# Performance work log

Hardware: AMD Instinct MI355X
Metric: run time of the kernel (lower is better)

Reference implementation:

```python
import jax, jax.numpy as jnp
import numpy as np

EPS = 1e-8  # torch CosineSimilarity default eps

def _normalize(x):
    # torch clamps each norm at eps before dividing
    n = jnp.sqrt(jnp.sum(x * x, axis=-1, keepdims=True))
    return x / jnp.maximum(n, EPS)

def _cross_entropy(logits, labels):
    logp = jax.nn.log_softmax(logits, axis=-1)
    return -jnp.mean(jnp.take_along_axis(logp, labels[:, None], axis=-1))

def setup_inputs() -> dict:
    key = jax.random.key(0)
    ks = jax.random.split(key, 7)
    B, M, D = 8192, 3129, 512
    return {
        'mm_proj': jax.random.normal(ks[0], (B, D), jnp.float32),
        'ans_embedding': jax.random.normal(ks[1], (M, D), jnp.float32),
        'v_max': jax.random.normal(ks[2], (B, D), jnp.float32),
        'mm': jax.random.normal(ks[3], (B, D), jnp.float32),
        'logits_q': jax.random.normal(ks[4], (B, M), jnp.float32),
        'logits_rubi': jax.random.normal(ks[5], (B, M), jnp.float32),
        'class_id': jax.random.randint(ks[6], (B, 1), 0, M, jnp.int64),
    }

def reference(mm_proj, ans_embedding, v_max, mm, logits_q, logits_rubi, class_id,
              question_loss_weight=1.0):
    cid = class_id.squeeze(1)  # [B]
    # NCE over cosine similarities: fuse normalize + GEMM instead of [B,M,D] expand
    g = _normalize(mm_proj)          # [B, D]
    a = _normalize(ans_embedding)    # [M, D]
    d_logit = jnp.einsum('bd,md->bm', g, a)  # [B, M] cosine matrix
    positive_dist = jnp.take_along_axis(d_logit, cid[:, None], axis=1)[:, 0]  # [B]
    num = jnp.exp(positive_dist)
    den = jnp.sum(jnp.exp(d_logit), axis=-1)
    loss_nce = jnp.mean(-jnp.log(num / den))
    # object cosine loss
    obj_dist = jnp.sum(_normalize(v_max) * _normalize(mm), axis=-1)  # [B]
    obj_loss = jnp.mean(1.0 - obj_dist)
    fusion_loss = (_cross_entropy(logits_rubi, cid) + obj_loss + loss_nce) / 3.0
    question_loss = _cross_entropy(logits_q, cid)
    loss = fusion_loss + question_loss_weight * question_loss
    # out['loss'], out['loss_mm_q'], out['loss_q']
    return jnp.stack([loss, fusion_loss, question_loss])
```

## Files before the change

kernel.cpp:

```cpp
#include <hip/hip_runtime.h>
#include <hip/hip_bf16.h>

#define B_N 8192
#define M_N 3129
#define M_PAD 3200
#define D_N 512

#define GLOBAL_AS __attribute__((address_space(1)))
#define LDS_AS __attribute__((address_space(3)))

typedef __bf16 bf16x8 __attribute__((ext_vector_type(8)));
typedef float f32x4 __attribute__((ext_vector_type(4)));

__global__ __launch_bounds__(256) void normalize_kernel(
    const float* __restrict__ x, __bf16* __restrict__ y,
    int nrows_src, int nrows_out) {
  int wid = threadIdx.x >> 6, lane = threadIdx.x & 63;
  int row = blockIdx.x * 4 + wid;
  if (row >= nrows_out) return;
  bf16x8 out;
  if (row >= nrows_src) {
    for (int j = 0; j < 8; ++j) out[j] = (__bf16)0.0f;
    *(bf16x8*)(y + (size_t)row * D_N + lane * 8) = out;
    return;
  }
  const float4* xr = (const float4*)(x + (size_t)row * D_N);
  float4 v0 = xr[lane * 2], v1 = xr[lane * 2 + 1];
  float s = v0.x*v0.x + v0.y*v0.y + v0.z*v0.z + v0.w*v0.w
          + v1.x*v1.x + v1.y*v1.y + v1.z*v1.z + v1.w*v1.w;
  for (int o = 1; o < 64; o <<= 1) s += __shfl_xor(s, o);
  float rn = 1.0f / fmaxf(sqrtf(s), 1e-8f);
  float vals[8] = {v0.x, v0.y, v0.z, v0.w, v1.x, v1.y, v1.z, v1.w};
  for (int j = 0; j < 8; ++j) out[j] = (__bf16)(vals[j] * rn);
  *(bf16x8*)(y + (size_t)row * D_N + lane * 8) = out;
}

__global__ __launch_bounds__(256) void pos_kernel(
    const __bf16* __restrict__ g, const __bf16* __restrict__ a,
    const int* __restrict__ cid, float* __restrict__ pos) {
  int wid = threadIdx.x >> 6, lane = threadIdx.x & 63;
  int b = blockIdx.x * 4 + wid;
  if (b >= B_N) return;
  int label = cid[b];
  bf16x8 gv = *(const bf16x8*)(g + (size_t)b * D_N + lane * 8);
  bf16x8 av = *(const bf16x8*)(a + (size_t)label * D_N + lane * 8);
  float s = 0.0f;
  for (int j = 0; j < 8; ++j) s += (float)gv[j] * (float)av[j];
  for (int o = 1; o < 64; o <<= 1) s += __shfl_xor(s, o);
  if (lane == 0) pos[b] = s;
}

__global__ __launch_bounds__(256) void nce_gemm_kernel(
    const __bf16* __restrict__ g, const __bf16* __restrict__ a,
    float* __restrict__ den) {
  __shared__ __bf16 As[128 * 32];
  __shared__ __bf16 Bs[128 * 32];
  const int t = threadIdx.x;
  const int mtile = blockIdx.x;
  const int btile = blockIdx.y;
  const int brow0 = btile * 128;
  const int mrow0 = mtile * 128;
  const int lane = t & 63;
  const int wid = t >> 6;
  const int wrow = wid >> 1;
  const int wcol = wid & 1;
  const int r = lane & 15;
  const int quad = lane >> 4;

  f32x4 acc[4][4];
  for (int i = 0; i < 4; ++i)
    for (int j = 0; j < 4; ++j)
      acc[i][j] = f32x4{0.f, 0.f, 0.f, 0.f};

  for (int k0 = 0; k0 < D_N; k0 += 32) {
    __syncthreads();
    for (int i = 0; i < 2; ++i) {
      int s = t + i * 256;
      int row = s >> 2;
      int kq = (s & 3) << 3;
      const __bf16* ga = g + (size_t)(brow0 + row) * D_N + (k0 + kq);
      __builtin_amdgcn_global_load_lds((const GLOBAL_AS void*)ga,
                                       (LDS_AS void*)(As + s * 8), 16, 0, 0);
      const __bf16* gb = a + (size_t)(mrow0 + row) * D_N + (k0 + kq);
      __builtin_amdgcn_global_load_lds((const GLOBAL_AS void*)gb,
                                       (LDS_AS void*)(Bs + s * 8), 16, 0, 0);
    }
    __syncthreads();
    bf16x8 af[4], bf[4];
    for (int i = 0; i < 4; ++i)
      af[i] = *(const bf16x8*)(As + (wrow * 64 + i * 16 + r) * 32 + quad * 8);
    for (int j = 0; j < 4; ++j)
      bf[j] = *(const bf16x8*)(Bs + (wcol * 64 + j * 16 + r) * 32 + quad * 8);
    for (int i = 0; i < 4; ++i)
      for (int j = 0; j < 4; ++j)
        acc[i][j] = __builtin_amdgcn_mfma_f32_16x16x32_bf16(af[i], bf[j],
                                                            acc[i][j], 0, 0, 0);
  }

  for (int i = 0; i < 4; ++i) {
    for (int reg = 0; reg < 4; ++reg) {
      float s = 0.0f;
      for (int j = 0; j < 4; ++j) {
        int m = mrow0 + wcol * 64 + j * 16 + r;
        float v = acc[i][j][reg];
        if (m < M_N) s += __expf(v);
      }
      s += __shfl_xor(s, 1);
      s += __shfl_xor(s, 2);
      s += __shfl_xor(s, 4);
      s += __shfl_xor(s, 8);
      if (r == 0) {
        int b = brow0 + wrow * 64 + i * 16 + quad * 4 + reg;
        atomicAdd(den + b, s);
      }
    }
  }
}

__global__ __launch_bounds__(256) void obj_kernel(
    const float* __restrict__ v, const float* __restrict__ m,
    float* __restrict__ obj) {
  int wid = threadIdx.x >> 6, lane = threadIdx.x & 63;
  int b = blockIdx.x * 4 + wid;
  if (b >= B_N) return;
  const float4* vr = (const float4*)(v + (size_t)b * D_N);
  const float4* mr = (const float4*)(m + (size_t)b * D_N);
  float4 a0 = vr[lane * 2], a1 = vr[lane * 2 + 1];
  float4 b0 = mr[lane * 2], b1 = mr[lane * 2 + 1];
  float sv = a0.x*a0.x + a0.y*a0.y + a0.z*a0.z + a0.w*a0.w
           + a1.x*a1.x + a1.y*a1.y + a1.z*a1.z + a1.w*a1.w;
  float sm = b0.x*b0.x + b0.y*b0.y + b0.z*b0.z + b0.w*b0.w
           + b1.x*b1.x + b1.y*b1.y + b1.z*b1.z + b1.w*b1.w;
  float sd = a0.x*b0.x + a0.y*b0.y + a0.z*b0.z + a0.w*b0.w
           + a1.x*b1.x + a1.y*b1.y + a1.z*b1.z + a1.w*b1.w;
  for (int o = 1; o < 64; o <<= 1) {
    sv += __shfl_xor(sv, o);
    sm += __shfl_xor(sm, o);
    sd += __shfl_xor(sd, o);
  }
  if (lane == 0) {
    float dist = sd / (fmaxf(sqrtf(sv), 1e-8f) * fmaxf(sqrtf(sm), 1e-8f));
    obj[b] = 1.0f - dist;
  }
}

__global__ __launch_bounds__(256) void ce_kernel(
    const float* __restrict__ lq, const float* __restrict__ lr,
    const int* __restrict__ cid,
    float* __restrict__ ce_q, float* __restrict__ ce_r) {
  int b = blockIdx.x;
  const float* rq = lq + (size_t)b * M_N;
  const float* rr = lr + (size_t)b * M_N;
  int t = threadIdx.x;
  int mis = (int)(((size_t)b * M_N) & 3);
  int h = (4 - mis) & 3;
  int n4 = (M_N - h) >> 2;
  int tail0 = h + (n4 << 2);
  int ntail = M_N - tail0;
  float sq = 0.0f, sr = 0.0f;
  if (t < h) { sq += __expf(rq[t]); sr += __expf(rr[t]); }
  if (t >= 64 && t < 64 + ntail) {
    int i = tail0 + (t - 64);
    sq += __expf(rq[i]); sr += __expf(rr[i]);
  }
  const float4* q4 = (const float4*)(rq + h);
  const float4* r4 = (const float4*)(rr + h);
  for (int i = t; i < n4; i += 256) {
    float4 a = q4[i];
    float4 c = r4[i];
    sq += __expf(a.x) + __expf(a.y) + __expf(a.z) + __expf(a.w);
    sr += __expf(c.x) + __expf(c.y) + __expf(c.z) + __expf(c.w);
  }
  for (int o = 1; o < 64; o <<= 1) {
    sq += __shfl_xor(sq, o);
    sr += __shfl_xor(sr, o);
  }
  __shared__ float ssq[4], ssr[4];
  int wid = t >> 6;
  if ((t & 63) == 0) { ssq[wid] = sq; ssr[wid] = sr; }
  __syncthreads();
  if (t == 0) {
    float tq = ssq[0] + ssq[1] + ssq[2] + ssq[3];
    float tr = ssr[0] + ssr[1] + ssr[2] + ssr[3];
    int label = cid[b];
    ce_q[b] = logf(tq) - rq[label];
    ce_r[b] = logf(tr) - rr[label];
  }
}

__global__ __launch_bounds__(256) void final_kernel(
    const float* __restrict__ den, const float* __restrict__ pos,
    const float* __restrict__ ce_q, const float* __restrict__ ce_r,
    const float* __restrict__ obj, float* __restrict__ out) {
  int t = threadIdx.x;
  float s_nce = 0.0f, s_ceq = 0.0f, s_cer = 0.0f, s_obj = 0.0f;
  for (int b = t; b < B_N; b += 256) {
    s_nce += logf(den[b]) - pos[b];
    s_ceq += ce_q[b];
    s_cer += ce_r[b];
    s_obj += obj[b];
  }
  for (int o = 1; o < 64; o <<= 1) {
    s_nce += __shfl_xor(s_nce, o);
    s_ceq += __shfl_xor(s_ceq, o);
    s_cer += __shfl_xor(s_cer, o);
    s_obj += __shfl_xor(s_obj, o);
  }
  __shared__ float red[4][4];
  int wid = t >> 6;
  if ((t & 63) == 0) {
    red[wid][0] = s_nce; red[wid][1] = s_ceq;
    red[wid][2] = s_cer; red[wid][3] = s_obj;
  }
  __syncthreads();
  if (t == 0) {
    float nce = (red[0][0] + red[1][0] + red[2][0] + red[3][0]) / (float)B_N;
    float ceq = (red[0][1] + red[1][1] + red[2][1] + red[3][1]) / (float)B_N;
    float cer = (red[0][2] + red[1][2] + red[2][2] + red[3][2]) / (float)B_N;
    float ob  = (red[0][3] + red[1][3] + red[2][3] + red[3][3]) / (float)B_N;
    float fusion = (cer + ob + nce) * (1.0f / 3.0f);
    float loss = fusion + ceq;
    out[0] = loss;
    out[1] = fusion;
    out[2] = ceq;
  }
}

extern "C" void kernel_launch(void* const* d_in, const int* in_sizes, int n_in,
                              void* d_out, int out_size, void* d_ws, size_t ws_size,
                              hipStream_t stream) {
  const float* mm_proj     = (const float*)d_in[0];
  const float* ans_emb     = (const float*)d_in[1];
  const float* v_max       = (const float*)d_in[2];
  const float* mm          = (const float*)d_in[3];
  const float* logits_q    = (const float*)d_in[4];
  const float* logits_rubi = (const float*)d_in[5];
  const int*   cid         = (const int*)d_in[6];
  float* out = (float*)d_out;

  char* ws = (char*)d_ws;
  __bf16* g = (__bf16*)ws;
  __bf16* a = (__bf16*)(ws + 8388608);
  float* den  = (float*)(ws + 8388608 + 3276800);
  float* pos  = den + B_N;
  float* ce_q = pos + B_N;
  float* ce_r = ce_q + B_N;
  float* obj  = ce_r + B_N;

  hipMemsetAsync(den, 0, (size_t)B_N * sizeof(float), stream);

  normalize_kernel<<<B_N / 4, 256, 0, stream>>>(mm_proj, g, B_N, B_N);
  normalize_kernel<<<M_PAD / 4, 256, 0, stream>>>(ans_emb, a, M_N, M_PAD);
  pos_kernel<<<B_N / 4, 256, 0, stream>>>(g, a, cid, pos);
  nce_gemm_kernel<<<dim3(M_PAD / 128, B_N / 128), 256, 0, stream>>>(g, a, den);
  obj_kernel<<<B_N / 4, 256, 0, stream>>>(v_max, mm, obj);
  ce_kernel<<<B_N, 256, 0, stream>>>(logits_q, logits_rubi, cid, ce_q, ce_r);
  final_kernel<<<1, 256, 0, stream>>>(den, pos, ce_q, ce_r, obj, out);
}
```

Before: 340.2 us.

## Fuse prep kernels, stage CE rows via LDS async loads, parallelize final reduction

Merges the two normalize launches and the object-cosine kernel into one prep kernel to cut launch count. Rewrites the cross-entropy kernel to copy each logits row into LDS with global_load_lds from an aligned start and mask the edges, replacing the scalar head/tail handling. Splits the single-block final reduction into a multi-block atomic reduce plus a tiny combine kernel. This adds two launches at the end, atomic float ordering nondeterminism, and heavy LDS use per CE block that may lower occupancy.

Result: faster. 325.1 us (-4.4%).

```diff
diff --git a/kernel.cpp b/kernel.cpp
--- a/kernel.cpp
+++ b/kernel.cpp
@@ -12,12 +12,13 @@
 typedef __bf16 bf16x8 __attribute__((ext_vector_type(8)));
 typedef float f32x4 __attribute__((ext_vector_type(4)));
 
-__global__ __launch_bounds__(256) void normalize_kernel(
+#define PREP_G_BLOCKS   (B_N / 4)
+#define PREP_A_BLOCKS   (M_PAD / 4)
+#define PREP_OBJ_BLOCKS (B_N / 4)
+
+__device__ __forceinline__ void normalize_row(
     const float* __restrict__ x, __bf16* __restrict__ y,
-    int nrows_src, int nrows_out) {
-  int wid = threadIdx.x >> 6, lane = threadIdx.x & 63;
-  int row = blockIdx.x * 4 + wid;
-  if (row >= nrows_out) return;
+    int row, int nrows_src, int lane) {
   bf16x8 out;
   if (row >= nrows_src) {
     for (int j = 0; j < 8; ++j) out[j] = (__bf16)0.0f;
@@ -33,6 +34,41 @@
   float vals[8] = {v0.x, v0.y, v0.z, v0.w, v1.x, v1.y, v1.z, v1.w};
   for (int j = 0; j < 8; ++j) out[j] = (__bf16)(vals[j] * rn);
   *(bf16x8*)(y + (size_t)row * D_N + lane * 8) = out;
+}
+
+__global__ __launch_bounds__(256) void prep_kernel(
+    const float* __restrict__ mm_proj, const float* __restrict__ ans_emb,
+    const float* __restrict__ v_max, const float* __restrict__ mm,
+    __bf16* __restrict__ g, __bf16* __restrict__ a,
+    float* __restrict__ obj) {
+  int blk = blockIdx.x;
+  int wid = threadIdx.x >> 6, lane = threadIdx.x & 63;
+  if (blk < PREP_G_BLOCKS) {
+    normalize_row(mm_proj, g, blk * 4 + wid, B_N, lane);
+  } else if (blk < PREP_G_BLOCKS + PREP_A_BLOCKS) {
+    normalize_row(ans_emb, a, (blk - PREP_G_BLOCKS) * 4 + wid, M_N, lane);
+  } else {
+    int b = (blk - PREP_G_BLOCKS - PREP_A_BLOCKS) * 4 + wid;
+    const float4* vr = (const float4*)(v_max + (size_t)b * D_N);
+    const float4* mr = (const float4*)(mm + (size_t)b * D_N);
+    float4 a0 = vr[lane * 2], a1 = vr[lane * 2 + 1];
+    float4 b0 = mr[lane * 2], b1 = mr[lane * 2 + 1];
+    float sv = a0.x*a0.x + a0.y*a0.y + a0.z*a0.z + a0.w*a0.w
+             + a1.x*a1.x + a1.y*a1.y + a1.z*a1.z + a1.w*a1.w;
+    float sm = b0.x*b0.x + b0.y*b0.y + b0.z*b0.z + b0.w*b0.w
+             + b1.x*b1.x + b1.y*b1.y + b1.z*b1.z + b1.w*b1.w;
+    float sd = a0.x*b0.x + a0.y*b0.y + a0.z*b0.z + a0.w*b0.w
+             + a1.x*b1.x + a1.y*b1.y + a1.z*b1.z + a1.w*b1.w;
+    for (int o = 1; o < 64; o <<= 1) {
+      sv += __shfl_xor(sv, o);
+      sm += __shfl_xor(sm, o);
+      sd += __shfl_xor(sd, o);
+    }
+    if (lane == 0) {
+      float dist = sd / (fmaxf(sqrtf(sv), 1e-8f) * fmaxf(sqrtf(sm), 1e-8f));
+      obj[b] = 1.0f - dist;
+    }
+  }
 }
 
 __global__ __launch_bounds__(256) void pos_kernel(
@@ -56,10 +92,8 @@
   __shared__ __bf16 As[128 * 32];
   __shared__ __bf16 Bs[128 * 32];
   const int t = threadIdx.x;
-  const int mtile = blockIdx.x;
-  const int btile = blockIdx.y;
-  const int brow0 = btile * 128;
-  const int mrow0 = mtile * 128;
+  const int brow0 = blockIdx.y * 128;
+  const int mrow0 = blockIdx.x * 128;
   const int lane = t & 63;
   const int wid = t >> 6;
   const int wrow = wid >> 1;
@@ -102,8 +136,7 @@
       float s = 0.0f;
       for (int j = 0; j < 4; ++j) {
         int m = mrow0 + wcol * 64 + j * 16 + r;
-        float v = acc[i][j][reg];
-        if (m < M_N) s += __expf(v);
+        if (m < M_N) s += __expf(acc[i][j][reg]);
       }
       s += __shfl_xor(s, 1);
       s += __shfl_xor(s, 2);
@@ -117,59 +150,55 @@
   }
 }
 
-__global__ __launch_bounds__(256) void obj_kernel(
-    const float* __restrict__ v, const float* __restrict__ m,
-    float* __restrict__ obj) {
-  int wid = threadIdx.x >> 6, lane = threadIdx.x & 63;
-  int b = blockIdx.x * 4 + wid;
-  if (b >= B_N) return;
-  const float4* vr = (const float4*)(v + (size_t)b * D_N);
-  const float4* mr = (const float4*)(m + (size_t)b * D_N);
-  float4 a0 = vr[lane * 2], a1 = vr[lane * 2 + 1];
-  float4 b0 = mr[lane * 2], b1 = mr[lane * 2 + 1];
-  float sv = a0.x*a0.x + a0.y*a0.y + a0.z*a0.z + a0.w*a0.w
-           + a1.x*a1.x + a1.y*a1.y + a1.z*a1.z + a1.w*a1.w;
-  float sm = b0.x*b0.x + b0.y*b0.y + b0.z*b0.z + b0.w*b0.w
-           + b1.x*b1.x + b1.y*b1.y + b1.z*b1.z + b1.w*b1.w;
-  float sd = a0.x*b0.x + a0.y*b0.y + a0.z*b0.z + a0.w*b0.w
-           + a1.x*b1.x + a1.y*b1.y + a1.z*b1.z + a1.w*b1.w;
-  for (int o = 1; o < 64; o <<= 1) {
-    sv += __shfl_xor(sv, o);
-    sm += __shfl_xor(sm, o);
-    sd += __shfl_xor(sd, o);
-  }
-  if (lane == 0) {
-    float dist = sd / (fmaxf(sqrtf(sv), 1e-8f) * fmaxf(sqrtf(sm), 1e-8f));
-    obj[b] = 1.0f - dist;
-  }
-}
+#define CE_CHUNKS 784
 
 __global__ __launch_bounds__(256) void ce_kernel(
     const float* __restrict__ lq, const float* __restrict__ lr,
     const int* __restrict__ cid,
     float* __restrict__ ce_q, float* __restrict__ ce_r) {
-  int b = blockIdx.x;
-  const float* rq = lq + (size_t)b * M_N;
-  const float* rr = lr + (size_t)b * M_N;
-  int t = threadIdx.x;
-  int mis = (int)(((size_t)b * M_N) & 3);
-  int h = (4 - mis) & 3;
-  int n4 = (M_N - h) >> 2;
-  int tail0 = h + (n4 << 2);
-  int ntail = M_N - tail0;
+  __shared__ float Lq[CE_CHUNKS * 4];
+  __shared__ float Lr[CE_CHUNKS * 4];
+  const int b = blockIdx.x;
+  const int t = threadIdx.x;
+  const size_t start = ((size_t)b * M_N) & ~(size_t)3;
+  const int mis = b & 3;
+  const size_t TOTAL = (size_t)B_N * M_N;
+
+#pragma unroll
+  for (int k = 0; k < 3; ++k) {
+    int c = t + k * 256;
+    size_t gi = start + (size_t)c * 4;
+    if (gi + 4 > TOTAL) gi = TOTAL - 4;
+    __builtin_amdgcn_global_load_lds((const GLOBAL_AS void*)(lq + gi),
+                                     (LDS_AS void*)(Lq + c * 4), 16, 0, 0);
+    __builtin_amdgcn_global_load_lds((const GLOBAL_AS void*)(lr + gi),
+                                     (LDS_AS void*)(Lr + c * 4), 16, 0, 0);
+  }
+  if (t < CE_CHUNKS - 768) {
+    int c = t + 768;
+    size_t gi = start + (size_t)c * 4;
+    if (gi + 4 > TOTAL) gi = TOTAL - 4;
+    __builtin_amdgcn_global_load_lds((const GLOBAL_AS void*)(lq + gi),
+                                     (LDS_AS void*)(Lq + c * 4), 16, 0, 0);
+    __builtin_amdgcn_global_load_lds((const GLOBAL_AS void*)(lr + gi),
+                                     (LDS_AS void*)(Lr + c * 4), 16, 0, 0);
+  }
+  __syncthreads();
+
+  const int lo = mis, hi = mis + M_N;
   float sq = 0.0f, sr = 0.0f;
-  if (t < h) { sq += __expf(rq[t]); sr += __expf(rr[t]); }
-  if (t >= 64 && t < 64 + ntail) {
-    int i = tail0 + (t - 64);
-    sq += __expf(rq[i]); sr += __expf(rr[i]);
-  }
-  const float4* q4 = (const float4*)(rq + h);
-  const float4* r4 = (const float4*)(rr + h);
-  for (int i = t; i < n4; i += 256) {
-    float4 a = q4[i];
-    float4 c = r4[i];
-    sq += __expf(a.x) + __expf(a.y) + __expf(a.z) + __expf(a.w);
-    sr += __expf(c.x) + __expf(c.y) + __expf(c.z) + __expf(c.w);
+#pragma unroll
+  for (int k = 0; k < 4; ++k) {
+    int c = t + k * 256;
+    if (c < CE_CHUNKS) {
+      float4 q = *(const float4*)(Lq + c * 4);
+      float4 p = *(const float4*)(Lr + c * 4);
+      int e = c * 4;
+      if (e + 0 >= lo && e + 0 < hi) { sq += __expf(q.x); sr += __expf(p.x); }
+      if (e + 1 >= lo && e + 1 < hi) { sq += __expf(q.y); sr += __expf(p.y); }
+      if (e + 2 >= lo && e + 2 < hi) { sq += __expf(q.z); sr += __expf(p.z); }
+      if (e + 3 >= lo && e + 3 < hi) { sq += __expf(q.w); sr += __expf(p.w); }
+    }
   }
   for (int o = 1; o < 64; o <<= 1) {
     sq += __shfl_xor(sq, o);
@@ -183,23 +212,20 @@
     float tq = ssq[0] + ssq[1] + ssq[2] + ssq[3];
     float tr = ssr[0] + ssr[1] + ssr[2] + ssr[3];
     int label = cid[b];
-    ce_q[b] = logf(tq) - rq[label];
-    ce_r[b] = logf(tr) - rr[label];
-  }
-}
-
-__global__ __launch_bounds__(256) void final_kernel(
+    ce_q[b] = logf(tq) - Lq[mis + label];
+    ce_r[b] = logf(tr) - Lr[mis + label];
+  }
+}
+
+__global__ __launch_bounds__(256) void final_reduce_kernel(
     const float* __restrict__ den, const float* __restrict__ pos,
     const float* __restrict__ ce_q, const float* __restrict__ ce_r,
-    const float* __restrict__ obj, float* __restrict__ out) {
-  int t = threadIdx.x;
-  float s_nce = 0.0f, s_ceq = 0.0f, s_cer = 0.0f, s_obj = 0.0f;
-  for (int b = t; b < B_N; b += 256) {
-    s_nce += logf(den[b]) - pos[b];
-    s_ceq += ce_q[b];
-    s_cer += ce_r[b];
-    s_obj += obj[b];
-  }
+    const float* __restrict__ obj, float* __restrict__ acc) {
+  int b = blockIdx.x * 256 + threadIdx.x;
+  float s_nce = logf(den[b]) - pos[b];
+  float s_ceq = ce_q[b];
+  float s_cer = ce_r[b];
+  float s_obj = obj[b];
   for (int o = 1; o < 64; o <<= 1) {
     s_nce += __shfl_xor(s_nce, o);
     s_ceq += __shfl_xor(s_ceq, o);
@@ -207,20 +233,28 @@
     s_obj += __shfl_xor(s_obj, o);
   }
   __shared__ float red[4][4];
-  int wid = t >> 6;
-  if ((t & 63) == 0) {
+  int wid = threadIdx.x >> 6;
+  if ((threadIdx.x & 63) == 0) {
     red[wid][0] = s_nce; red[wid][1] = s_ceq;
     red[wid][2] = s_cer; red[wid][3] = s_obj;
   }
   __syncthreads();
-  if (t == 0) {
-    float nce = (red[0][0] + red[1][0] + red[2][0] + red[3][0]) / (float)B_N;
-    float ceq = (red[0][1] + red[1][1] + red[2][1] + red[3][1]) / (float)B_N;
-    float cer = (red[0][2] + red[1][2] + red[2][2] + red[3][2]) / (float)B_N;
-    float ob  = (red[0][3] + red[1][3] + red[2][3] + red[3][3]) / (float)B_N;
+  if (threadIdx.x < 4) {
+    float v = red[0][threadIdx.x] + red[1][threadIdx.x]
+            + red[2][threadIdx.x] + red[3][threadIdx.x];
+    atomicAdd(acc + threadIdx.x, v);
+  }
+}
+
+__global__ void final_combine_kernel(const float* __restrict__ acc,
+                                     float* __restrict__ out) {
+  if (threadIdx.x == 0) {
+    float nce = acc[0] / (float)B_N;
+    float ceq = acc[1] / (float)B_N;
+    float cer = acc[2] / (float)B_N;
+    float ob  = acc[3] / (float)B_N;
     float fusion = (cer + ob + nce) * (1.0f / 3.0f);
-    float loss = fusion + ceq;
-    out[0] = loss;
+    out[0] = fusion + ceq;
     out[1] = fusion;
     out[2] = ceq;
   }
@@ -242,18 +276,20 @@
   __bf16* g = (__bf16*)ws;
   __bf16* a = (__bf16*)(ws + 8388608);
   float* den  = (float*)(ws + 8388608 + 3276800);
-  float* pos  = den + B_N;
+  float* acc  = den + B_N;
+  float* pos  = acc + 4;
   float* ce_q = pos + B_N;
   float* ce_r = ce_q + B_N;
   float* obj  = ce_r + B_N;
 
-  hipMemsetAsync(den, 0, (size_t)B_N * sizeof(float), stream);
-
-  normalize_kernel<<<B_N / 4, 256, 0, stream>>>(mm_proj, g, B_N, B_N);
-  normalize_kernel<<<M_PAD / 4, 256, 0, stream>>>(ans_emb, a, M_N, M_PAD);
+  hipMemsetAsync(den, 0, (size_t)(B_N + 4) * sizeof(float), stream);
+
+  prep_kernel<<<PREP_G_BLOCKS + PREP_A_BLOCKS + PREP_OBJ_BLOCKS, 256, 0,
+                stream>>>(mm_proj, ans_emb, v_max, mm, g, a, obj);
   pos_kernel<<<B_N / 4, 256, 0, stream>>>(g, a, cid, pos);
   nce_gemm_kernel<<<dim3(M_PAD / 128, B_N / 128), 256, 0, stream>>>(g, a, den);
-  obj_kernel<<<B_N / 4, 256, 0, stream>>>(v_max, mm, obj);
   ce_kernel<<<B_N, 256, 0, stream>>>(logits_q, logits_rubi, cid, ce_q, ce_r);
-  final_kernel<<<1, 256, 0, stream>>>(den, pos, ce_q, ce_r, obj, out);
-}
+  final_reduce_kernel<<<B_N / 256, 256, 0, stream>>>(den, pos, ce_q, ce_r,
+                                                     obj, acc);
+  final_combine_kernel<<<1, 64, 0, stream>>>(acc, out);
+}
```
